# Performance work log

Hardware: AMD Instinct MI355X
Metric: run time of the kernel (lower is better)

Reference implementation:

```python
import jax, jax.numpy as jnp
import numpy as np

E = 16          # total experts (two halves of 8)
E_HALF = 8
K = 2           # top-k per token
CAP_FACTOR = 2  # expert capacity factor over the average load


def setup_inputs() -> dict:
    key = jax.random.key(0)
    ks = jax.random.split(key, 6)
    N, D, F = 16384, 1024, 1024  # tokens, d_model, d_ff (repo uses d_ff == d_model)
    s = 0.02
    return {
        "moe_inp": jax.random.normal(ks[0], (N, D), jnp.float32),
        "gate_w": jax.random.normal(ks[1], (D, E), jnp.float32) * s,   # gate Linear(d_model, 16)
        "gate_b": jnp.zeros((E,), jnp.float32),
        "route_w": jax.random.normal(ks[2], (D, 1), jnp.float32) * s,  # self.weights Linear(d_model, 1)
        "route_b": jnp.zeros((1,), jnp.float32),
        "W1": jax.random.normal(ks[3], (E, D, F), jnp.float32) * s,    # htoh4 per expert
        "b1": jnp.zeros((E, F), jnp.float32),
        "W2": jax.random.normal(ks[4], (E, F, D), jnp.float32) * s,    # h4toh per expert
        "b2": jnp.zeros((E, D), jnp.float32),
    }


def reference(moe_inp, gate_w, gate_b, route_w, route_b, W1, b1, W2, b2):
    N, D = moe_inp.shape
    # --- gate: logits over 16 experts; half 1 -> experts [0,8), half 2 -> experts [8,16)
    logits = moe_inp @ gate_w + gate_b                       # [N, E]
    val1, idx1 = jax.lax.top_k(logits[:, :E_HALF], K)        # [N, K]
    score1 = jax.nn.softmax(val1, axis=-1)
    val2, idx2 = jax.lax.top_k(logits[:, E_HALF:], K)
    score2 = jax.nn.softmax(val2, axis=-1)
    idx2 = idx2 + E_HALF                                     # shift into second expert range (gate_top_k_idx_2 + 8)
    # --- hard binary split of tokens via sigmoid(Linear(d,1)) > 0.5
    group1 = jax.nn.sigmoid(moe_inp @ route_w + route_b) > 0.5   # [N, 1]
    idx = jnp.where(group1, idx1, idx2)                      # [N, K] combined routing
    score = jnp.where(group1, score1, score2)                # [N, K]
    # --- dispatch: flatten (token, slot) pairs, capacity-bucket per expert
    T = N * K
    C = CAP_FACTOR * T // E                                  # expert capacity
    flat_idx = idx.reshape(-1)                               # [T]
    flat_x = jnp.repeat(moe_inp, K, axis=0)                  # [T, D]
    onehot = jax.nn.one_hot(flat_idx, E, dtype=jnp.int32)    # [T, E]
    pos_in_e = (jnp.cumsum(onehot, axis=0) * onehot).sum(axis=1) - 1  # [T] slot within expert
    valid = pos_in_e < C
    safe_pos = jnp.where(valid, pos_in_e, 0)
    buf = jnp.zeros((E, C, D), moe_inp.dtype).at[flat_idx, safe_pos].add(
        jnp.where(valid[:, None], flat_x, 0.0))              # [E, C, D] contiguous per-expert inputs
    # --- grouped expert FFN: relu(x W1 + b1) W2 + b2 (dropout = identity in eval)
    h = jax.nn.relu(jnp.einsum('ecd,edf->ecf', buf, W1) + b1[:, None, :])
    y = jnp.einsum('ecf,efd->ecd', h, W2) + b2[:, None, :]   # [E, C, D]
    # --- gather back and combine with gate scores
    y_flat = jnp.where(valid[:, None], y[flat_idx, safe_pos], 0.0)   # [T, D]
    out = (y_flat.reshape(N, K, D) * score[..., None]).sum(axis=1)   # [N, D]
    return out
```

## Files before the change

kernel.cpp:

```cpp
#include <hip/hip_runtime.h>
#include <hip/hip_bf16.h>
#include <stdint.h>

#define N_TOK 16384
#define DMODEL 1024
#define EXP 16
#define CAP 4096
#define TT 32768

typedef __bf16 bf16x8 __attribute__((ext_vector_type(8)));
typedef __bf16 bf16x4 __attribute__((ext_vector_type(4)));
typedef float  f32x4  __attribute__((ext_vector_type(4)));

__device__ __forceinline__ void gl_lds16(const void* g, void* s) {
  __builtin_amdgcn_global_load_lds(
      (__attribute__((address_space(1))) void*)(void*)g,
      (__attribute__((address_space(3))) void*)s, 16, 0, 0);
}

__device__ __forceinline__ float bfbits2f(unsigned short u) {
  return __uint_as_float(((unsigned)u) << 16);
}

#define FENCE asm volatile("" ::: "memory")
#define BAR() do { FENCE; __builtin_amdgcn_s_barrier(); FENCE; } while (0)

__global__ __launch_bounds__(256) void prep_kernel(const float* __restrict__ W1,
                                                   const float* __restrict__ W2,
                                                   __bf16* __restrict__ W1bt,
                                                   __bf16* __restrict__ W2bt,
                                                   const float* __restrict__ x,
                                                   const float* __restrict__ gw,
                                                   const float* __restrict__ gb,
                                                   const float* __restrict__ rw,
                                                   const float* __restrict__ rb,
                                                   int* __restrict__ idxo,
                                                   float* __restrict__ sco,
                                                   __bf16* __restrict__ Xb) {
  __shared__ char smem[21504];
  int bid = blockIdx.x;
  int tid = threadIdx.x;
  if (bid % 9 != 8) {
    int cb = bid - (bid + 1) / 9;
    float (*tile)[65] = (float(*)[65])smem;
    int tx = cb & 15;
    int ty = (cb >> 4) & 15;
    int e  = (cb >> 8) & 15;
    int which = (cb >> 12) & 1;
    const float* src = (which ? W2 : W1) + (size_t)e * DMODEL * DMODEL;
    __bf16*      dst = (which ? W2bt : W1bt) + (size_t)e * DMODEL * DMODEL;
    int r = tid >> 2;
    int cs = (tid & 3) * 16;
    int r0 = ty * 64, c0 = tx * 64;
    #pragma unroll
    for (int i = 0; i < 16; i += 4) {
      float4 v = *(const float4*)(src + (size_t)(r0 + r) * DMODEL + c0 + cs + i);
      tile[r][cs + i + 0] = v.x; tile[r][cs + i + 1] = v.y;
      tile[r][cs + i + 2] = v.z; tile[r][cs + i + 3] = v.w;
    }
    __syncthreads();
    bf16x8 o1, o2;
    #pragma unroll
    for (int i = 0; i < 8; i++) o1[i] = (__bf16)tile[cs + i][r];
    #pragma unroll
    for (int i = 0; i < 8; i++) o2[i] = (__bf16)tile[cs + 8 + i][r];
    *(bf16x8*)(dst + (size_t)(c0 + r) * DMODEL + r0 + cs)     = o1;
    *(bf16x8*)(dst + (size_t)(c0 + r) * DMODEL + r0 + cs + 8) = o2;
  } else {
    float* gws = (float*)smem;
    float* rws = (float*)(smem + 20480);
    int g = bid / 9;
    int w = tid >> 6, lane = tid & 63;
    int n0t = g * 16 + w * 4;
    const float* xr0 = x + (size_t)(n0t + 0) * DMODEL;
    const float* xr1 = x + (size_t)(n0t + 1) * DMODEL;
    const float* xr2 = x + (size_t)(n0t + 2) * DMODEL;
    const float* xr3 = x + (size_t)(n0t + 3) * DMODEL;

    float acc0[17], acc1[17], acc2[17], acc3[17];
    #pragma unroll
    for (int j = 0; j < 17; j++) { acc0[j] = 0.f; acc1[j] = 0.f; acc2[j] = 0.f; acc3[j] = 0.f; }

    for (int c = 0; c < 4; c++) {
      int c0 = c * 256;
      __syncthreads();
      #pragma unroll
      for (int q = tid, it = 0; it < 4; q += 256, it++) {
        float4 v = *(const float4*)(gw + c0 * 16 + q * 4);
        *(float4*)(gws + (q >> 2) * 20 + (q & 3) * 4) = v;
      }
      rws[tid] = rw[c0 + tid];
      __syncthreads();

      #pragma unroll
      for (int dv = 0; dv < 4; dv++) {
        int dl = dv * 64 + lane;
        int d  = c0 + dl;
        float x0 = xr0[d], x1 = xr1[d], x2 = xr2[d], x3 = xr3[d];
        Xb[(size_t)(n0t + 0) * DMODEL + d] = (__bf16)x0;
        Xb[(size_t)(n0t + 1) * DMODEL + d] = (__bf16)x1;
        Xb[(size_t)(n0t + 2) * DMODEL + d] = (__bf16)x2;
        Xb[(size_t)(n0t + 3) * DMODEL + d] = (__bf16)x3;
        const float* gp = gws + dl * 20;
        float4 g0 = *(const float4*)(gp);
        float4 g1 = *(const float4*)(gp + 4);
        float4 g2 = *(const float4*)(gp + 8);
        float4 g3 = *(const float4*)(gp + 12);
        float rv = rws[dl];
        float gj[16] = {g0.x, g0.y, g0.z, g0.w, g1.x, g1.y, g1.z, g1.w,
                        g2.x, g2.y, g2.z, g2.w, g3.x, g3.y, g3.z, g3.w};
        #pragma unroll
        for (int j = 0; j < 16; j++) {
          acc0[j] += x0 * gj[j]; acc1[j] += x1 * gj[j];
          acc2[j] += x2 * gj[j]; acc3[j] += x3 * gj[j];
        }
        acc0[16] += x0 * rv; acc1[16] += x1 * rv;
        acc2[16] += x2 * rv; acc3[16] += x3 * rv;
      }
    }

    #pragma unroll
    for (int o = 1; o < 64; o <<= 1) {
      #pragma unroll
      for (int j = 0; j < 17; j++) {
        acc0[j] += __shfl_xor(acc0[j], o);
        acc1[j] += __shfl_xor(acc1[j], o);
        acc2[j] += __shfl_xor(acc2[j], o);
        acc3[j] += __shfl_xor(acc3[j], o);
      }
    }
    if (lane == 0) {
      float* accs[4] = {acc0, acc1, acc2, acc3};
      #pragma unroll
      for (int tk = 0; tk < 4; tk++) {
        float* acc = accs[tk];
        int n = n0t + tk;
        float rv = acc[16] + rb[0];
        bool g1f = rv > 0.f;
        float c[8];
        #pragma unroll
        for (int j = 0; j < 8; j++)
          c[j] = (g1f ? acc[j] + gb[j] : acc[8 + j] + gb[8 + j]);
        int i1 = 0; float v1 = c[0];
        #pragma unroll
        for (int j = 1; j < 8; j++) { if (c[j] > v1) { v1 = c[j]; i1 = j; } }
        int i2 = -1; float v2 = -3.4e38f;
        #pragma unroll
        for (int j = 0; j < 8; j++) { if (j != i1 && c[j] > v2) { v2 = c[j]; i2 = j; } }
        float e2 = expf(v2 - v1);
        float den = 1.f + e2;
        int base = g1f ? 0 : 8;
        idxo[2 * n] = base + i1; idxo[2 * n + 1] = base + i2;
        sco[2 * n] = 1.f / den;  sco[2 * n + 1] = e2 / den;
      }
    }
  }
}

__global__ __launch_bounds__(1024) void scan_kernel(const int* __restrict__ idx,
                                                    float* __restrict__ sco,
                                                    int* __restrict__ rowlist,
                                                    int* __restrict__ cnt,
                                                    int* __restrict__ off) {
  __shared__ int hist[16 * 1024];
  int tid = threadIdx.x;
  #pragma unroll
  for (int e = 0; e < 16; e++) hist[e * 1024 + tid] = 0;
  __syncthreads();
  int base = tid * 32;
  for (int i = 0; i < 32; i++) {
    int e = idx[base + i];
    hist[e * 1024 + tid]++;
  }
  __syncthreads();
  int w = tid >> 6, lane = tid & 63;
  {
    int e = w;
    int running = 0;
    for (int cch = 0; cch < 16; cch++) {
      int v = hist[e * 1024 + cch * 64 + lane];
      int orig = v;
      #pragma unroll
      for (int o = 1; o < 64; o <<= 1) {
        int nv = __shfl_up(v, o);
        if (lane >= o) v += nv;
      }
      hist[e * 1024 + cch * 64 + lane] = running + v - orig;
      running += __shfl(v, 63);
    }
    if (lane == 0) cnt[e] = running;
  }
  __syncthreads();
  if (tid == 0) {
    int o = 0;
    for (int e = 0; e < 16; e++) {
      int c = cnt[e]; if (c > CAP) c = CAP;
      off[e] = o; cnt[e] = c; o += c;
    }
  }
  __syncthreads();
  for (int i = 0; i < 32; i++) {
    int t = base + i;
    int e = idx[t];
    int r = hist[e * 1024 + tid]++;
    if (r < CAP) rowlist[e * CAP + r] = t;
    else sco[t] = 0.f;
  }
}

#define GBM 128
#define GBN 128
#define GBK 64
#define NKT (DMODEL / GBK)

__global__ __launch_bounds__(256, 2) void moe_gemm(const __bf16* __restrict__ A,
                                                   const __bf16* __restrict__ Bt,
                                                   const float* __restrict__ bias,
                                                   __bf16* __restrict__ out,
                                                   const int* __restrict__ rowlist,
                                                   const int* __restrict__ cnt,
                                                   const int* __restrict__ off,
                                                   int mode) {
  __shared__ char lds[65536];
  int bx = blockIdx.x;
  int em = (bx & 7) * 64 + (bx >> 3);
  int e  = em >> 5;
  int m0 = (em & 31) * GBM;
  int ce = cnt[e];
  if (m0 >= ce) return;
  int n0 = blockIdx.y * GBN;
  int oe = off[e];
  int tid = threadIdx.x;

  const __bf16* aP[4];
  const __bf16* bP[4];
  #pragma unroll
  for (int j = 0; j < 4; j++) {
    int c = j * 256 + tid;
    int srow = c >> 3;
    int gsrc = (c & 7) ^ (srow & 7);
    int rr = m0 + srow; if (rr > ce - 1) rr = ce - 1;
    size_t arow;
    if (mode == 0) arow = (size_t)(rowlist[e * CAP + rr] >> 1);
    else           arow = (size_t)(oe + rr);
    aP[j] = A + arow * DMODEL + gsrc * 8;
    bP[j] = Bt + (size_t)e * DMODEL * DMODEL + (size_t)(n0 + srow) * DMODEL + gsrc * 8;
  }

  int w = tid >> 6, lane = tid & 63;
  int wr = (w >> 1) * 64;
  int wc = (w & 1) * 64;
  int fr = lane & 15, fg = lane >> 4;

  int aRd = wr * 128 + fr * 128;
  int bRd = 32768 + wc * 128 + fr * 128;
  int gk0 = ((fg)     ^ (fr & 7)) * 16;
  int gk1 = ((4 | fg) ^ (fr & 7)) * 16;

  f32x4 acc[4][4];
  #pragma unroll
  for (int mi = 0; mi < 4; mi++)
    #pragma unroll
    for (int ni = 0; ni < 4; ni++)
      #pragma unroll
      for (int l = 0; l < 4; l++) acc[mi][ni][l] = 0.f;

  auto stA = [&](int s) {
    char* dst = lds + (s & 1) * 16384;
    #pragma unroll
    for (int j = 0; j < 4; j++)
      gl_lds16(aP[j] + s * 64, dst + (size_t)(j * 256 + tid) * 16);
  };
  auto stB = [&](int s) {
    char* dst = lds + 32768 + (s & 1) * 16384;
    #pragma unroll
    for (int j = 0; j < 4; j++)
      gl_lds16(bP[j] + s * 64, dst + (size_t)(j * 256 + tid) * 16);
  };

  stA(0); stB(0); stA(1); stB(1);
  asm volatile("s_waitcnt vmcnt(8)" ::: "memory");
  BAR();

  bf16x8 afA[4][2], bq0[2][2], bq1[2][2];
  for (int t = 0; t < NKT; ++t) {
    const char* Ab = lds + (t & 1) * 16384 + aRd;
    const char* Bb = lds + (t & 1) * 16384 + bRd;

    #pragma unroll
    for (int mi = 0; mi < 4; mi++) {
      afA[mi][0] = *(const bf16x8*)(Ab + mi * 2048 + gk0);
      afA[mi][1] = *(const bf16x8*)(Ab + mi * 2048 + gk1);
    }
    #pragma unroll
    for (int ni = 0; ni < 2; ni++) {
      bq0[ni][0] = *(const bf16x8*)(Bb + ni * 2048 + gk0);
      bq0[ni][1] = *(const bf16x8*)(Bb + ni * 2048 + gk1);
      bq1[ni][0] = *(const bf16x8*)(Bb + (2 + ni) * 2048 + gk0);
      bq1[ni][1] = *(const bf16x8*)(Bb + (2 + ni) * 2048 + gk1);
    }
    asm volatile("s_waitcnt lgkmcnt(0)" ::: "memory");
    __builtin_amdgcn_sched_barrier(0);
    __builtin_amdgcn_s_setprio(1);
    #pragma unroll
    for (int kk = 0; kk < 2; kk++)
      #pragma unroll
      for (int mi = 0; mi < 4; mi++)
        #pragma unroll
        for (int ni = 0; ni < 2; ni++)
          acc[mi][ni] = __builtin_amdgcn_mfma_f32_16x16x32_bf16(afA[mi][kk], bq0[ni][kk], acc[mi][ni], 0, 0, 0);
    __builtin_amdgcn_s_setprio(0);
    BAR();

    if (t <= NKT - 3) { stA(t + 2); stB(t + 2); }
    __builtin_amdgcn_s_setprio(1);
    #pragma unroll
    for (int kk = 0; kk < 2; kk++)
      #pragma unroll
      for (int mi = 0; mi < 4; mi++)
        #pragma unroll
        for (int ni = 0; ni < 2; ni++)
          acc[mi][2 + ni] = __builtin_amdgcn_mfma_f32_16x16x32_bf16(afA[mi][kk], bq1[ni][kk], acc[mi][2 + ni], 0, 0, 0);
    __builtin_amdgcn_s_setprio(0);
    if (t <= NKT - 3)      asm volatile("s_waitcnt vmcnt(8)" ::: "memory");
    else if (t == NKT - 2) asm volatile("s_waitcnt vmcnt(0)" ::: "memory");
    BAR();
  }

  float bcol[4];
  #pragma unroll
  for (int ni = 0; ni < 4; ni++)
    bcol[ni] = bias[(size_t)e * DMODEL + n0 + wc + ni * 16 + fr];
  #pragma unroll
  for (int mi = 0; mi < 4; mi++) {
    #pragma unroll
    for (int r = 0; r < 4; r++) {
      int grow = m0 + wr + mi * 16 + fg * 4 + r;
      if (grow >= ce) continue;
      size_t orow = (mode == 0) ? (size_t)(oe + grow)
                                : (size_t)rowlist[e * CAP + grow];
      __bf16* op = out + orow * DMODEL + n0 + wc + fr;
      #pragma unroll
      for (int ni = 0; ni < 4; ni++) {
        float v = acc[mi][ni][r] + bcol[ni];
        if (mode == 0) v = fmaxf(v, 0.f);
        op[ni * 16] = (__bf16)v;
      }
    }
  }
}

__global__ __launch_bounds__(256) void combine_kernel(const __bf16* __restrict__ y,
                                                      const float* __restrict__ sco,
                                                      float* __restrict__ out) {
  int n = blockIdx.x;
  int d = threadIdx.x * 4;
  float s0 = sco[2 * n], s1 = sco[2 * n + 1];
  ushort4 a = *(const ushort4*)((const unsigned short*)(y + (size_t)(2 * n) * DMODEL + d));
  ushort4 b = *(const ushort4*)((const unsigned short*)(y + (size_t)(2 * n + 1) * DMODEL + d));
  float4 o;
  o.x = s0 * bfbits2f(a.x) + s1 * bfbits2f(b.x);
  o.y = s0 * bfbits2f(a.y) + s1 * bfbits2f(b.y);
  o.z = s0 * bfbits2f(a.z) + s1 * bfbits2f(b.z);
  o.w = s0 * bfbits2f(a.w) + s1 * bfbits2f(b.w);
  *(float4*)(out + (size_t)n * DMODEL + d) = o;
}

extern "C" void kernel_launch(void* const* d_in, const int* in_sizes, int n_in,
                              void* d_out, int out_size, void* d_ws, size_t ws_size,
                              hipStream_t stream) {
  const float* moe = (const float*)d_in[0];
  const float* gw  = (const float*)d_in[1];
  const float* gb  = (const float*)d_in[2];
  const float* rw  = (const float*)d_in[3];
  const float* rb  = (const float*)d_in[4];
  const float* W1  = (const float*)d_in[5];
  const float* b1  = (const float*)d_in[6];
  const float* W2  = (const float*)d_in[7];
  const float* b2  = (const float*)d_in[8];
  float* out = (float*)d_out;

  char* p = (char*)d_ws;
  __bf16* Xb   = (__bf16*)p; p += (size_t)N_TOK * DMODEL * 2;
  __bf16* W1bt = (__bf16*)p; p += (size_t)EXP * DMODEL * DMODEL * 2;
  __bf16* W2bt = (__bf16*)p; p += (size_t)EXP * DMODEL * DMODEL * 2;
  __bf16* hbuf = (__bf16*)p; p += (size_t)TT * DMODEL * 2;
  __bf16* ybuf = (__bf16*)p; p += (size_t)TT * DMODEL * 2;
  int*   idxb   = (int*)p;   p += (size_t)TT * 4;
  float* scoreb = (float*)p; p += (size_t)TT * 4;
  int*   rowlist = (int*)p;  p += (size_t)EXP * CAP * 4;
  int*   cntb    = (int*)p;  p += 64;
  int*   offb    = (int*)p;  p += 64;

  prep_kernel<<<dim3(9216), dim3(256), 0, stream>>>(W1, W2, W1bt, W2bt,
                                                    moe, gw, gb, rw, rb,
                                                    idxb, scoreb, Xb);
  scan_kernel<<<dim3(1), dim3(1024), 0, stream>>>(idxb, scoreb, rowlist, cntb, offb);
  moe_gemm<<<dim3(512, 8), dim3(256), 0, stream>>>(Xb, W1bt, b1, hbuf, rowlist, cntb, offb, 0);
  moe_gemm<<<dim3(512, 8), dim3(256), 0, stream>>>(hbuf, W2bt, b2, ybuf, rowlist, cntb, offb, 1);
  combine_kernel<<<dim3(16384), dim3(256), 0, stream>>>(ybuf, scoreb, out);
}
```

Measured before the change: 367.3 us.

## Pre-swizzle expert weights into MFMA fragment layout and load B directly to registers

The weight-conversion pass now writes the transposed bf16 weights in a fragment-major layout that matches the 16x16x32 MFMA B operand. The GEMM then loads B fragments from global memory straight into registers, double-buffered one k-step ahead, and no longer stages B through LDS. This halves LDS use and removes B's LDS writes and reads, which could improve occupancy. In exchange it raises register pressure and relies on global-load latency being hidden by the register prefetch, with vmcnt counts retuned to match.

```diff
diff --git a/kernel.cpp b/kernel.cpp
--- a/kernel.cpp
+++ b/kernel.cpp
@@ -64,8 +64,16 @@
     for (int i = 0; i < 8; i++) o1[i] = (__bf16)tile[cs + i][r];
     #pragma unroll
     for (int i = 0; i < 8; i++) o2[i] = (__bf16)tile[cs + 8 + i][r];
-    *(bf16x8*)(dst + (size_t)(c0 + r) * DMODEL + r0 + cs)     = o1;
-    *(bf16x8*)(dst + (size_t)(c0 + r) * DMODEL + r0 + cs + 8) = o2;
+    {
+      int n  = c0 + r;
+      int g  = n >> 4, fr = n & 15;
+      int k1 = r0 + cs;
+      int c1 = k1 >> 5, fg1 = (k1 >> 3) & 3;
+      int k2 = k1 + 8;
+      int c2 = k2 >> 5, fg2 = (k2 >> 3) & 3;
+      *(bf16x8*)(dst + ((size_t)(g * 32 + c1) * 512 + (fg1 * 16 + fr) * 8)) = o1;
+      *(bf16x8*)(dst + ((size_t)(g * 32 + c2) * 512 + (fg2 * 16 + fr) * 8)) = o2;
+    }
   } else {
     float* gws = (float*)smem;
     float* rws = (float*)(smem + 20480);
@@ -214,14 +222,14 @@
 #define NKT (DMODEL / GBK)
 
 __global__ __launch_bounds__(256, 2) void moe_gemm(const __bf16* __restrict__ A,
-                                                   const __bf16* __restrict__ Bt,
+                                                   const __bf16* __restrict__ Bf,
                                                    const float* __restrict__ bias,
                                                    __bf16* __restrict__ out,
                                                    const int* __restrict__ rowlist,
                                                    const int* __restrict__ cnt,
                                                    const int* __restrict__ off,
                                                    int mode) {
-  __shared__ char lds[65536];
+  __shared__ char lds[32768];
   int bx = blockIdx.x;
   int em = (bx & 7) * 64 + (bx >> 3);
   int e  = em >> 5;
@@ -233,7 +241,6 @@
   int tid = threadIdx.x;
 
   const __bf16* aP[4];
-  const __bf16* bP[4];
   #pragma unroll
   for (int j = 0; j < 4; j++) {
     int c = j * 256 + tid;
@@ -244,7 +251,6 @@
     if (mode == 0) arow = (size_t)(rowlist[e * CAP + rr] >> 1);
     else           arow = (size_t)(oe + rr);
     aP[j] = A + arow * DMODEL + gsrc * 8;
-    bP[j] = Bt + (size_t)e * DMODEL * DMODEL + (size_t)(n0 + srow) * DMODEL + gsrc * 8;
   }
 
   int w = tid >> 6, lane = tid & 63;
@@ -253,9 +259,12 @@
   int fr = lane & 15, fg = lane >> 4;
 
   int aRd = wr * 128 + fr * 128;
-  int bRd = 32768 + wc * 128 + fr * 128;
   int gk0 = ((fg)     ^ (fr & 7)) * 16;
   int gk1 = ((4 | fg) ^ (fr & 7)) * 16;
+
+  const __bf16* bF = Bf + (size_t)e * DMODEL * DMODEL
+                        + (size_t)(((n0 + wc) >> 4) * 32) * 512
+                        + (size_t)lane * 8;
 
   f32x4 acc[4][4];
   #pragma unroll
@@ -271,60 +280,63 @@
     for (int j = 0; j < 4; j++)
       gl_lds16(aP[j] + s * 64, dst + (size_t)(j * 256 + tid) * 16);
   };
-  auto stB = [&](int s) {
-    char* dst = lds + 32768 + (s & 1) * 16384;
-    #pragma unroll
-    for (int j = 0; j < 4; j++)
-      gl_lds16(bP[j] + s * 64, dst + (size_t)(j * 256 + tid) * 16);
+
+  bf16x8 bqA[4][2], bqB[4][2];
+
+  auto ldB = [&](int s, bf16x8 (&dst)[4][2]) {
+    #pragma unroll
+    for (int ni = 0; ni < 4; ni++) {
+      dst[ni][0] = *(const bf16x8*)(bF + ni * 16384 + (2 * s) * 512);
+      dst[ni][1] = *(const bf16x8*)(bF + ni * 16384 + (2 * s + 1) * 512);
+    }
   };
 
-  stA(0); stB(0); stA(1); stB(1);
-  asm volatile("s_waitcnt vmcnt(8)" ::: "memory");
+  ldB(0, bqA);
+  FENCE;
+  stA(0); stA(1);
+  asm volatile("s_waitcnt vmcnt(4)" ::: "memory");
   BAR();
 
-  bf16x8 afA[4][2], bq0[2][2], bq1[2][2];
-  for (int t = 0; t < NKT; ++t) {
-    const char* Ab = lds + (t & 1) * 16384 + aRd;
-    const char* Bb = lds + (t & 1) * 16384 + bRd;
-
+  bf16x8 afA[4][2];
+
+  auto giter = [&](int T, bf16x8 (&cur)[4][2], bf16x8 (&nxt)[4][2]) {
+    const char* Ab = lds + (T & 1) * 16384 + aRd;
     #pragma unroll
     for (int mi = 0; mi < 4; mi++) {
       afA[mi][0] = *(const bf16x8*)(Ab + mi * 2048 + gk0);
       afA[mi][1] = *(const bf16x8*)(Ab + mi * 2048 + gk1);
     }
-    #pragma unroll
-    for (int ni = 0; ni < 2; ni++) {
-      bq0[ni][0] = *(const bf16x8*)(Bb + ni * 2048 + gk0);
-      bq0[ni][1] = *(const bf16x8*)(Bb + ni * 2048 + gk1);
-      bq1[ni][0] = *(const bf16x8*)(Bb + (2 + ni) * 2048 + gk0);
-      bq1[ni][1] = *(const bf16x8*)(Bb + (2 + ni) * 2048 + gk1);
-    }
+    if (T + 1 < NKT) ldB(T + 1, nxt);
     asm volatile("s_waitcnt lgkmcnt(0)" ::: "memory");
     __builtin_amdgcn_sched_barrier(0);
     __builtin_amdgcn_s_setprio(1);
     #pragma unroll
     for (int kk = 0; kk < 2; kk++)
       #pragma unroll
-      for (int mi = 0; mi < 4; mi++)
-        #pragma unroll
-        for (int ni = 0; ni < 2; ni++)
-          acc[mi][ni] = __builtin_amdgcn_mfma_f32_16x16x32_bf16(afA[mi][kk], bq0[ni][kk], acc[mi][ni], 0, 0, 0);
+      for (int mi = 0; mi < 4; mi++) {
+        acc[mi][0] = __builtin_amdgcn_mfma_f32_16x16x32_bf16(afA[mi][kk], cur[0][kk], acc[mi][0], 0, 0, 0);
+        acc[mi][1] = __builtin_amdgcn_mfma_f32_16x16x32_bf16(afA[mi][kk], cur[1][kk], acc[mi][1], 0, 0, 0);
+      }
     __builtin_amdgcn_s_setprio(0);
     BAR();
-
-    if (t <= NKT - 3) { stA(t + 2); stB(t + 2); }
+    if (T <= NKT - 3) stA(T + 2);
     __builtin_amdgcn_s_setprio(1);
     #pragma unroll
     for (int kk = 0; kk < 2; kk++)
       #pragma unroll
-      for (int mi = 0; mi < 4; mi++)
-        #pragma unroll
-        for (int ni = 0; ni < 2; ni++)
-          acc[mi][2 + ni] = __builtin_amdgcn_mfma_f32_16x16x32_bf16(afA[mi][kk], bq1[ni][kk], acc[mi][2 + ni], 0, 0, 0);
+      for (int mi = 0; mi < 4; mi++) {
+        acc[mi][2] = __builtin_amdgcn_mfma_f32_16x16x32_bf16(afA[mi][kk], cur[2][kk], acc[mi][2], 0, 0, 0);
+        acc[mi][3] = __builtin_amdgcn_mfma_f32_16x16x32_bf16(afA[mi][kk], cur[3][kk], acc[mi][3], 0, 0, 0);
+      }
     __builtin_amdgcn_s_setprio(0);
-    if (t <= NKT - 3)      asm volatile("s_waitcnt vmcnt(8)" ::: "memory");
-    else if (t == NKT - 2) asm volatile("s_waitcnt vmcnt(0)" ::: "memory");
+    if (T <= NKT - 3)      asm volatile("s_waitcnt vmcnt(12)" ::: "memory");
+    else if (T == NKT - 2) asm volatile("s_waitcnt vmcnt(8)" ::: "memory");
     BAR();
+  };
+
+  for (int tt = 0; tt < NKT; tt += 2) {
+    giter(tt, bqA, bqB);
+    giter(tt + 1, bqB, bqA);
   }
 
   float bcol[4];
```

Result: slower. 388.1 us (+5.7%).
